# Performance work log

Measured on AMD Instinct MI355X. Metric: run time of the kernel, lower is better.

Reference implementation:

```python
import jax, jax.numpy as jnp
import numpy as np

BETA = 0.25  # commitment_beta from CodebookDecoder default


def setup_inputs() -> dict:
    key = jax.random.key(0)
    k1, k2, k3 = jax.random.split(key, 3)
    Q, B, K, D = 2048, 40000, 2048, 512
    return {
        "query_emb": jax.random.normal(k1, (Q, D), dtype=jnp.float32),
        "entity_emb": jax.random.normal(k2, (B, D), dtype=jnp.float32),
        "codebook": jax.random.normal(k3, (K, D), dtype=jnp.float32),
    }


def _quantize(x, codebook):
    # Nearest-neighbor lookup. torch.norm(x[:,None]-cb[None]) argmin is
    # equivalent to argmin of squared distance, expanded to avoid the
    x2 = jnp.sum(x * x, axis=1, keepdims=True)            # (B, 1)
    c2 = jnp.sum(codebook * codebook, axis=1)             # (K,)
    d2 = x2 - 2.0 * (x @ codebook.T) + c2[None, :]        # (B, K)
    idx = jnp.argmin(d2, axis=1)                          # (B,)
    quant = codebook[idx]                                 # (B, D) gather
    # vq_loss = mse(quant.detach(), x) + beta * mse(quant, x.detach())
    vq_loss = jnp.mean((jax.lax.stop_gradient(quant) - x) ** 2) \
        + BETA * jnp.mean((quant - jax.lax.stop_gradient(x)) ** 2)
    return quant, idx, vq_loss


def reference(query_emb, entity_emb, codebook):
    quant, idx, vq_loss = _quantize(entity_emb, codebook)
    score = query_emb @ quant.T                           # (Q, B)
    return score, vq_loss, idx
```

## Files before the change

kernel.cpp:

```cpp
#include <hip/hip_runtime.h>
#include <stdint.h>

#define Q    2048
#define NB   40000
#define NK   2048
#define ND   512
#define SCORE_SIZE (Q * NB)

typedef __bf16 bf16;
typedef bf16  bf16x8 __attribute__((ext_vector_type(8)));
typedef float f32x4  __attribute__((ext_vector_type(4)));

__device__ __forceinline__ unsigned short f2bf_rne(float f) {
    unsigned int u = __float_as_uint(f);
    u += 0x7FFFu + ((u >> 16) & 1u);
    return (unsigned short)(u >> 16);
}
__device__ __forceinline__ float bf2f(unsigned short h) {
    return __uint_as_float((unsigned int)h << 16);
}
__device__ __forceinline__ void split_pair_trunc(float x0, float x1,
                                                 unsigned int& hp, unsigned int& lp) {
    unsigned int u0 = __float_as_uint(x0), u1 = __float_as_uint(x1);
    hp = (u0 >> 16) | (u1 & 0xFFFF0000u);
    float l0 = x0 - __uint_as_float(u0 & 0xFFFF0000u);
    float l1 = x1 - __uint_as_float(u1 & 0xFFFF0000u);
    lp = (__float_as_uint(l0) >> 16) | (__float_as_uint(l1) & 0xFFFF0000u);
}

__global__ __launch_bounds__(256) void c2_kernel(const float* __restrict__ cb,
                                                 float* __restrict__ c2) {
    int wave = threadIdx.x >> 6, lane = threadIdx.x & 63;
    int row  = blockIdx.x * 4 + wave;
    const float4* p = (const float4*)(cb + (size_t)row * ND);
    float4 a = p[lane];
    float4 b = p[lane + 64];
    float s = a.x*a.x + a.y*a.y + a.z*a.z + a.w*a.w
            + b.x*b.x + b.y*b.y + b.z*b.z + b.w*b.w;
    #pragma unroll
    for (int off = 32; off; off >>= 1) s += __shfl_down(s, off);
    if (lane == 0) c2[row] = s;
}

__global__ __launch_bounds__(256) void cvt_cb_kernel(const float* __restrict__ cb,
        unsigned short* __restrict__ chi, unsigned short* __restrict__ clo) {
    int i = (blockIdx.x * 256 + threadIdx.x) * 4;
    float4 v = *(const float4*)(cb + i);
    unsigned short h[4]; float l[4];
    float x[4] = {v.x, v.y, v.z, v.w};
    #pragma unroll
    for (int j = 0; j < 4; ++j) { h[j] = f2bf_rne(x[j]); l[j] = x[j] - bf2f(h[j]); }
    uint2 hp, lp;
    hp.x = (unsigned int)h[0] | ((unsigned int)h[1] << 16);
    hp.y = (unsigned int)h[2] | ((unsigned int)h[3] << 16);
    lp.x = (unsigned int)f2bf_rne(l[0]) | ((unsigned int)f2bf_rne(l[1]) << 16);
    lp.y = (unsigned int)f2bf_rne(l[2]) | ((unsigned int)f2bf_rne(l[3]) << 16);
    *(uint2*)(chi + i) = hp;
    *(uint2*)(clo + i) = lp;
}

__global__ __launch_bounds__(256) void cvt_ent_kernel(const float* __restrict__ ent,
        unsigned short* __restrict__ ehi, unsigned short* __restrict__ elo) {
    int i = (blockIdx.x * 256 + threadIdx.x) * 4;
    float4 v = *(const float4*)(ent + i);
    unsigned short h[4]; float l[4];
    float x[4] = {v.x, v.y, v.z, v.w};
    #pragma unroll
    for (int j = 0; j < 4; ++j) { h[j] = f2bf_rne(x[j]); l[j] = x[j] - bf2f(h[j]); }
    uint2 hp, lp;
    hp.x = (unsigned int)h[0] | ((unsigned int)h[1] << 16);
    hp.y = (unsigned int)h[2] | ((unsigned int)h[3] << 16);
    lp.x = (unsigned int)f2bf_rne(l[0]) | ((unsigned int)f2bf_rne(l[1]) << 16);
    lp.y = (unsigned int)f2bf_rne(l[2]) | ((unsigned int)f2bf_rne(l[3]) << 16);
    *(uint2*)(ehi + i) = hp;
    *(uint2*)(elo + i) = lp;
}

__device__ __forceinline__ void top2_insert(float& v1, int& i1, float& v2, int& i2,
                                            float w, int j) {
    if (w < v1 || (w == v1 && j < i1)) { v2 = v1; i2 = i1; v1 = w; i1 = j; }
    else if (w < v2 || (w == v2 && j < i2)) { v2 = w; i2 = j; }
}

template<bool PRE>
__global__ __launch_bounds__(256) void dist_mfma_kernel(
        const float* __restrict__ entf,
        const unsigned short* __restrict__ ehi, const unsigned short* __restrict__ elo,
        const unsigned short* __restrict__ chi, const unsigned short* __restrict__ clo,
        const float* __restrict__ c2g, float4* __restrict__ partial) {
    __shared__ unsigned short EH[128 * 32];
    __shared__ unsigned short EL[128 * 32];
    __shared__ unsigned short CH[128 * 32];
    __shared__ unsigned short CL[128 * 32];
    int tid = threadIdx.x;
    int b0 = blockIdx.x * 128;
    int k0 = blockIdx.y * 128;
    int lane = tid & 63, wave = tid >> 6;
    int wm = wave >> 1, wn = wave & 1;
    int lr = lane & 15, quad = lane >> 4;

    f32x4 acc[4][4] = {};

    for (int kt = 0; kt < ND; kt += 32) {
        __syncthreads();
        #pragma unroll
        for (int r = 0; r < 2; ++r) {
            int e = r * 256 + tid;
            int row = e >> 2, cc = e & 3;
            int br = b0 + row; br = br < NB ? br : NB - 1;
            size_t eoff = (size_t)br * ND + kt + cc * 8;
            if (PRE) {
                *(uint4*)(EH + row * 32 + cc * 8) = *(const uint4*)(ehi + eoff);
                *(uint4*)(EL + row * 32 + cc * 8) = *(const uint4*)(elo + eoff);
            } else {
                const float* src = entf + eoff;
                float4 a = *(const float4*)src;
                float4 b = *(const float4*)(src + 4);
                uint4 hp, lp;
                split_pair_trunc(a.x, a.y, hp.x, lp.x);
                split_pair_trunc(a.z, a.w, hp.y, lp.y);
                split_pair_trunc(b.x, b.y, hp.z, lp.z);
                split_pair_trunc(b.z, b.w, hp.w, lp.w);
                *(uint4*)(EH + row * 32 + cc * 8) = hp;
                *(uint4*)(EL + row * 32 + cc * 8) = lp;
            }
            size_t coff = (size_t)(k0 + row) * ND + kt + cc * 8;
            *(uint4*)(CH + row * 32 + cc * 8) = *(const uint4*)(chi + coff);
            *(uint4*)(CL + row * 32 + cc * 8) = *(const uint4*)(clo + coff);
        }
        __syncthreads();
        bf16x8 ah[4], al[4], bh[4], bl[4];
        #pragma unroll
        for (int mi = 0; mi < 4; ++mi) {
            int o = (wm * 64 + mi * 16 + lr) * 32 + quad * 8;
            ah[mi] = *(const bf16x8*)(EH + o);
            al[mi] = *(const bf16x8*)(EL + o);
        }
        #pragma unroll
        for (int ni = 0; ni < 4; ++ni) {
            int o = (wn * 64 + ni * 16 + lr) * 32 + quad * 8;
            bh[ni] = *(const bf16x8*)(CH + o);
            bl[ni] = *(const bf16x8*)(CL + o);
        }
        #pragma unroll
        for (int mi = 0; mi < 4; ++mi)
            #pragma unroll
            for (int ni = 0; ni < 4; ++ni) {
                acc[mi][ni] = __builtin_amdgcn_mfma_f32_16x16x32_bf16(
                    ah[mi], bh[ni], acc[mi][ni], 0, 0, 0);
                acc[mi][ni] = __builtin_amdgcn_mfma_f32_16x16x32_bf16(
                    ah[mi], bl[ni], acc[mi][ni], 0, 0, 0);
                acc[mi][ni] = __builtin_amdgcn_mfma_f32_16x16x32_bf16(
                    al[mi], bh[ni], acc[mi][ni], 0, 0, 0);
            }
    }

    float c2v[4];
    #pragma unroll
    for (int ni = 0; ni < 4; ++ni) c2v[ni] = c2g[k0 + wn * 64 + ni * 16 + lr];

    #pragma unroll
    for (int mi = 0; mi < 4; ++mi) {
        #pragma unroll
        for (int rr = 0; rr < 4; ++rr) {
            float v1 = 3.4e38f, v2 = 3.4e38f;
            int i1 = 0x7FFFFFFF, i2 = 0x7FFFFFFF;
            #pragma unroll
            for (int ni = 0; ni < 4; ++ni) {
                float w = c2v[ni] - 2.0f * acc[mi][ni][rr];
                top2_insert(v1, i1, v2, i2, w, k0 + wn * 64 + ni * 16 + lr);
            }
            #pragma unroll
            for (int off = 1; off < 16; off <<= 1) {
                float ov1 = __shfl_xor(v1, off); int oi1 = __shfl_xor(i1, off);
                float ov2 = __shfl_xor(v2, off); int oi2 = __shfl_xor(i2, off);
                top2_insert(v1, i1, v2, i2, ov1, oi1);
                top2_insert(v1, i1, v2, i2, ov2, oi2);
            }
            int b = b0 + wm * 64 + mi * 16 + quad * 4 + rr;
            if (lr == 0 && b < NB)
                partial[(size_t)(blockIdx.y * 2 + wn) * NB + b] =
                    make_float4(v1, __int_as_float(i1), v2, __int_as_float(i2));
        }
    }
}

__global__ __launch_bounds__(256) void cand_merge_kernel(
        const float4* __restrict__ partial, int* __restrict__ cand) {
    int b = blockIdx.x * 256 + threadIdx.x;
    if (b >= NB) return;
    float tv[4] = {3.4e38f, 3.4e38f, 3.4e38f, 3.4e38f};
    int   ti[4] = {0x7FFFFFFF, 0x7FFFFFFF, 0x7FFFFFFF, 0x7FFFFFFF};
    for (int g = 0; g < 32; ++g) {
        float4 p = partial[(size_t)g * NB + b];
        float pv[2] = {p.x, p.z};
        int   pi[2] = {__float_as_int(p.y), __float_as_int(p.w)};
        #pragma unroll
        for (int t = 0; t < 2; ++t) {
            float w = pv[t]; int j = pi[t];
            #pragma unroll
            for (int s = 0; s < 4; ++s) {
                if (w < tv[s] || (w == tv[s] && j < ti[s])) {
                    float tmpv = tv[s]; int tmpi = ti[s];
                    tv[s] = w; ti[s] = j; w = tmpv; j = tmpi;
                }
            }
        }
    }
    #pragma unroll
    for (int s = 0; s < 4; ++s) cand[b * 4 + s] = ti[s];
}

__global__ __launch_bounds__(256) void rescore_kernel(
        const float* __restrict__ ent, const float* __restrict__ cb,
        const float* __restrict__ c2g, const int* __restrict__ cand,
        unsigned short* __restrict__ quantb, float* __restrict__ out_idx,
        float* __restrict__ acc) {
    int b = blockIdx.x;
    int wave = threadIdx.x >> 6, lane = threadIdx.x & 63;
    int k = cand[b * 4 + wave];
    const float4* xp = (const float4*)(ent + (size_t)b * ND);
    const float4* cp = (const float4*)(cb + (size_t)k * ND);
    float4 x0 = xp[lane * 2], x1 = xp[lane * 2 + 1];
    float4 c0 = cp[lane * 2], c1 = cp[lane * 2 + 1];
    float s = x0.x*c0.x + x0.y*c0.y + x0.z*c0.z + x0.w*c0.w
            + x1.x*c1.x + x1.y*c1.y + x1.z*c1.z + x1.w*c1.w;
    #pragma unroll
    for (int off = 32; off; off >>= 1) s += __shfl_down(s, off);
    __shared__ float vws[4];
    __shared__ int   kws[4];
    __shared__ int   win;
    if (lane == 0) { vws[wave] = c2g[k] - 2.0f * s; kws[wave] = k; }
    __syncthreads();
    if (threadIdx.x == 0) {
        float bv = vws[0]; int bk = kws[0], bw = 0;
        #pragma unroll
        for (int w = 1; w < 4; ++w) {
            if (vws[w] < bv || (vws[w] == bv && kws[w] < bk)) {
                bv = vws[w]; bk = kws[w]; bw = w;
            }
        }
        win = bw;
        out_idx[b] = (float)bk;
    }
    __syncthreads();
    if (wave == win) {
        uint4 qp;
        qp.x = (unsigned int)f2bf_rne(c0.x) | ((unsigned int)f2bf_rne(c0.y) << 16);
        qp.y = (unsigned int)f2bf_rne(c0.z) | ((unsigned int)f2bf_rne(c0.w) << 16);
        qp.z = (unsigned int)f2bf_rne(c1.x) | ((unsigned int)f2bf_rne(c1.y) << 16);
        qp.w = (unsigned int)f2bf_rne(c1.z) | ((unsigned int)f2bf_rne(c1.w) << 16);
        *(uint4*)(quantb + (size_t)b * ND + lane * 8) = qp;
        float d0 = c0.x - x0.x, d1 = c0.y - x0.y, d2 = c0.z - x0.z, d3 = c0.w - x0.w;
        float d4 = c1.x - x1.x, d5 = c1.y - x1.y, d6 = c1.z - x1.z, d7 = c1.w - x1.w;
        float l = d0*d0 + d1*d1 + d2*d2 + d3*d3 + d4*d4 + d5*d5 + d6*d6 + d7*d7;
        #pragma unroll
        for (int off = 32; off; off >>= 1) l += __shfl_down(l, off);
        if (lane == 0) atomicAdd(acc, l);
    }
}

__global__ void vq_final_kernel(const float* __restrict__ acc, float* __restrict__ out) {
    out[0] = 1.25f * acc[0] / (float)(NB * ND);
}

__global__ __launch_bounds__(256) void qcvt_kernel(const float* __restrict__ qry,
                                                   unsigned short* __restrict__ qb) {
    int i = (blockIdx.x * 256 + threadIdx.x) * 4;
    float4 v = *(const float4*)(qry + i);
    uint2 u;
    u.x = (unsigned int)f2bf_rne(v.x) | ((unsigned int)f2bf_rne(v.y) << 16);
    u.y = (unsigned int)f2bf_rne(v.z) | ((unsigned int)f2bf_rne(v.w) << 16);
    *(uint2*)(qb + i) = u;
}

__global__ __launch_bounds__(256) void score_kernel(
        const unsigned short* __restrict__ Aq, const unsigned short* __restrict__ Bq,
        float* __restrict__ C) {
    __shared__ unsigned short As[128 * 32];
    __shared__ unsigned short Bs[128 * 32];
    int tid = threadIdx.x;
    int n0 = blockIdx.x * 128;
    int m0 = blockIdx.y * 128;
    int lane = tid & 63, wave = tid >> 6;
    int wm = wave >> 1, wn = wave & 1;
    int lr = lane & 15, quad = lane >> 4;

    f32x4 acc[4][4] = {};

    for (int kt = 0; kt < ND; kt += 32) {
        __syncthreads();
        #pragma unroll
        for (int r = 0; r < 2; ++r) {
            int e = r * 256 + tid;
            int row = e >> 2, cc = e & 3;
            uint4 va = *(const uint4*)(Aq + (size_t)(m0 + row) * ND + kt + cc * 8);
            *(uint4*)(As + row * 32 + cc * 8) = va;
            int nr = n0 + row; nr = nr < NB ? nr : NB - 1;
            uint4 vb = *(const uint4*)(Bq + (size_t)nr * ND + kt + cc * 8);
            *(uint4*)(Bs + row * 32 + cc * 8) = vb;
        }
        __syncthreads();
        bf16x8 af[4], bfr[4];
        #pragma unroll
        for (int mi = 0; mi < 4; ++mi)
            af[mi] = *(const bf16x8*)(As + (wm * 64 + mi * 16 + lr) * 32 + quad * 8);
        #pragma unroll
        for (int ni = 0; ni < 4; ++ni)
            bfr[ni] = *(const bf16x8*)(Bs + (wn * 64 + ni * 16 + lr) * 32 + quad * 8);
        #pragma unroll
        for (int mi = 0; mi < 4; ++mi)
            #pragma unroll
            for (int ni = 0; ni < 4; ++ni)
                acc[mi][ni] = __builtin_amdgcn_mfma_f32_16x16x32_bf16(
                    af[mi], bfr[ni], acc[mi][ni], 0, 0, 0);
    }

    #pragma unroll
    for (int mi = 0; mi < 4; ++mi) {
        #pragma unroll
        for (int ni = 0; ni < 4; ++ni) {
            int col = n0 + wn * 64 + ni * 16 + lr;
            if (col < NB) {
                #pragma unroll
                for (int r = 0; r < 4; ++r) {
                    int row = m0 + wm * 64 + mi * 16 + quad * 4 + r;
                    C[(size_t)row * NB + col] = acc[mi][ni][r];
                }
            }
        }
    }
}

extern "C" void kernel_launch(void* const* d_in, const int* in_sizes, int n_in,
                              void* d_out, int out_size, void* d_ws, size_t ws_size,
                              hipStream_t stream) {
    const float* qry = (const float*)d_in[0];
    const float* ent = (const float*)d_in[1];
    const float* cb  = (const float*)d_in[2];
    float* out = (float*)d_out;

    char* ws = (char*)d_ws;
    const bool pre = ws_size >= 130ull * 1024 * 1024;

    float4*         partial = (float4*)(ws);
    unsigned short* quantb  = (unsigned short*)(ws);
    size_t off = 40960000;
    unsigned short *ehi = nullptr, *elo = nullptr;
    if (pre) {
        ehi = (unsigned short*)(ws + off); off += 40960000;
        elo = (unsigned short*)(ws + off); off += 40960000;
    }
    unsigned short* chi = (unsigned short*)(ws + off); off += 2097152;
    unsigned short* clo = (unsigned short*)(ws + off); off += 2097152;
    unsigned short* qb  = (unsigned short*)(ws + off); off += 2097152;
    int*            cand= (int*)(ws + off);            off += 640000;
    float*          c2  = (float*)(ws + off);          off += 8192;
    float*          acc = (float*)(ws + off);          off += 4;

    hipMemsetAsync(acc, 0, sizeof(float), stream);

    c2_kernel<<<NK / 4, 256, 0, stream>>>(cb, c2);
    cvt_cb_kernel<<<1024, 256, 0, stream>>>(cb, chi, clo);
    qcvt_kernel<<<1024, 256, 0, stream>>>(qry, qb);
    if (pre) {
        cvt_ent_kernel<<<20000, 256, 0, stream>>>(ent, ehi, elo);
        dist_mfma_kernel<true><<<dim3(313, 16), 256, 0, stream>>>(
            ent, ehi, elo, chi, clo, c2, partial);
    } else {
        dist_mfma_kernel<false><<<dim3(313, 16), 256, 0, stream>>>(
            ent, nullptr, nullptr, chi, clo, c2, partial);
    }
    cand_merge_kernel<<<(NB + 255) / 256, 256, 0, stream>>>(partial, cand);
    rescore_kernel<<<NB, 256, 0, stream>>>(ent, cb, c2, cand, quantb,
                                           out + SCORE_SIZE + 1, acc);
    vq_final_kernel<<<1, 1, 0, stream>>>(acc, out + SCORE_SIZE);
    score_kernel<<<dim3(313, 16), 256, 0, stream>>>(qb, quantb, out);
}
```

Baseline: 2.100 ms.

## Use single bf16 distance GEMM with wider rescoring and direct global-to-LDS loads

The distance GEMM drops the 3-pass split-bf16 scheme (hi/lo) in favour of one bf16 pass, which cuts its MFMA work and its memory traffic to about a third. To make up for the lower precision, candidate merging keeps the top 8 instead of the top 4, and these are rescored exactly in fp32 with 512-thread blocks. Both GEMMs now use K-tiles of 64, XOR-swizzled LDS layouts and global_load_lds DMA, which skips the trip through registers. The risk is argmin mismatches wherever the true nearest code falls outside the bf16 top-8.

```diff
diff --git a/kernel.cpp b/kernel.cpp
--- a/kernel.cpp
+++ b/kernel.cpp
@@ -16,16 +16,11 @@
     u += 0x7FFFu + ((u >> 16) & 1u);
     return (unsigned short)(u >> 16);
 }
-__device__ __forceinline__ float bf2f(unsigned short h) {
-    return __uint_as_float((unsigned int)h << 16);
-}
-__device__ __forceinline__ void split_pair_trunc(float x0, float x1,
-                                                 unsigned int& hp, unsigned int& lp) {
-    unsigned int u0 = __float_as_uint(x0), u1 = __float_as_uint(x1);
-    hp = (u0 >> 16) | (u1 & 0xFFFF0000u);
-    float l0 = x0 - __uint_as_float(u0 & 0xFFFF0000u);
-    float l1 = x1 - __uint_as_float(u1 & 0xFFFF0000u);
-    lp = (__float_as_uint(l0) >> 16) | (__float_as_uint(l1) & 0xFFFF0000u);
+
+__device__ __forceinline__ void gl2lds16(const void* g, void* l) {
+    __builtin_amdgcn_global_load_lds(
+        (const __attribute__((address_space(1))) void*)g,
+        (__attribute__((address_space(3))) void*)l, 16, 0, 0);
 }
 
 __global__ __launch_bounds__(256) void c2_kernel(const float* __restrict__ cb,
@@ -42,38 +37,14 @@
     if (lane == 0) c2[row] = s;
 }
 
-__global__ __launch_bounds__(256) void cvt_cb_kernel(const float* __restrict__ cb,
-        unsigned short* __restrict__ chi, unsigned short* __restrict__ clo) {
+__global__ __launch_bounds__(256) void cvt_bf16_kernel(const float* __restrict__ src,
+                                                       unsigned short* __restrict__ dst) {
     int i = (blockIdx.x * 256 + threadIdx.x) * 4;
-    float4 v = *(const float4*)(cb + i);
-    unsigned short h[4]; float l[4];
-    float x[4] = {v.x, v.y, v.z, v.w};
-    #pragma unroll
-    for (int j = 0; j < 4; ++j) { h[j] = f2bf_rne(x[j]); l[j] = x[j] - bf2f(h[j]); }
-    uint2 hp, lp;
-    hp.x = (unsigned int)h[0] | ((unsigned int)h[1] << 16);
-    hp.y = (unsigned int)h[2] | ((unsigned int)h[3] << 16);
-    lp.x = (unsigned int)f2bf_rne(l[0]) | ((unsigned int)f2bf_rne(l[1]) << 16);
-    lp.y = (unsigned int)f2bf_rne(l[2]) | ((unsigned int)f2bf_rne(l[3]) << 16);
-    *(uint2*)(chi + i) = hp;
-    *(uint2*)(clo + i) = lp;
-}
-
-__global__ __launch_bounds__(256) void cvt_ent_kernel(const float* __restrict__ ent,
-        unsigned short* __restrict__ ehi, unsigned short* __restrict__ elo) {
-    int i = (blockIdx.x * 256 + threadIdx.x) * 4;
-    float4 v = *(const float4*)(ent + i);
-    unsigned short h[4]; float l[4];
-    float x[4] = {v.x, v.y, v.z, v.w};
-    #pragma unroll
-    for (int j = 0; j < 4; ++j) { h[j] = f2bf_rne(x[j]); l[j] = x[j] - bf2f(h[j]); }
-    uint2 hp, lp;
-    hp.x = (unsigned int)h[0] | ((unsigned int)h[1] << 16);
-    hp.y = (unsigned int)h[2] | ((unsigned int)h[3] << 16);
-    lp.x = (unsigned int)f2bf_rne(l[0]) | ((unsigned int)f2bf_rne(l[1]) << 16);
-    lp.y = (unsigned int)f2bf_rne(l[2]) | ((unsigned int)f2bf_rne(l[3]) << 16);
-    *(uint2*)(ehi + i) = hp;
-    *(uint2*)(elo + i) = lp;
+    float4 v = *(const float4*)(src + i);
+    uint2 u;
+    u.x = (unsigned int)f2bf_rne(v.x) | ((unsigned int)f2bf_rne(v.y) << 16);
+    u.y = (unsigned int)f2bf_rne(v.z) | ((unsigned int)f2bf_rne(v.w) << 16);
+    *(uint2*)(dst + i) = u;
 }
 
 __device__ __forceinline__ void top2_insert(float& v1, int& i1, float& v2, int& i2,
@@ -84,14 +55,11 @@
 
 template<bool PRE>
 __global__ __launch_bounds__(256) void dist_mfma_kernel(
-        const float* __restrict__ entf,
-        const unsigned short* __restrict__ ehi, const unsigned short* __restrict__ elo,
-        const unsigned short* __restrict__ chi, const unsigned short* __restrict__ clo,
+        const float* __restrict__ entf, const unsigned short* __restrict__ ehi,
+        const unsigned short* __restrict__ chi,
         const float* __restrict__ c2g, float4* __restrict__ partial) {
-    __shared__ unsigned short EH[128 * 32];
-    __shared__ unsigned short EL[128 * 32];
-    __shared__ unsigned short CH[128 * 32];
-    __shared__ unsigned short CL[128 * 32];
+    __shared__ unsigned short Es[128 * 64];
+    __shared__ unsigned short Cs[128 * 64];
     int tid = threadIdx.x;
     int b0 = blockIdx.x * 128;
     int k0 = blockIdx.y * 128;
@@ -101,58 +69,54 @@
 
     f32x4 acc[4][4] = {};
 
-    for (int kt = 0; kt < ND; kt += 32) {
+    for (int kt = 0; kt < ND; kt += 64) {
         __syncthreads();
         #pragma unroll
-        for (int r = 0; r < 2; ++r) {
-            int e = r * 256 + tid;
-            int row = e >> 2, cc = e & 3;
-            int br = b0 + row; br = br < NB ? br : NB - 1;
-            size_t eoff = (size_t)br * ND + kt + cc * 8;
+        for (int j = 0; j < 4; ++j) {
+            int q = j * 256 + tid;
+            int r = q >> 3;
+            int cs = (q & 7) ^ (r & 7);
+            gl2lds16(chi + (size_t)(k0 + r) * ND + kt + cs * 8,
+                     Cs + (size_t)(j * 256 + wave * 64) * 8);
+            int br = b0 + r; br = br < NB ? br : NB - 1;
             if (PRE) {
-                *(uint4*)(EH + row * 32 + cc * 8) = *(const uint4*)(ehi + eoff);
-                *(uint4*)(EL + row * 32 + cc * 8) = *(const uint4*)(elo + eoff);
+                gl2lds16(ehi + (size_t)br * ND + kt + cs * 8,
+                         Es + (size_t)(j * 256 + wave * 64) * 8);
             } else {
-                const float* src = entf + eoff;
-                float4 a = *(const float4*)src;
-                float4 b = *(const float4*)(src + 4);
-                uint4 hp, lp;
-                split_pair_trunc(a.x, a.y, hp.x, lp.x);
-                split_pair_trunc(a.z, a.w, hp.y, lp.y);
-                split_pair_trunc(b.x, b.y, hp.z, lp.z);
-                split_pair_trunc(b.z, b.w, hp.w, lp.w);
-                *(uint4*)(EH + row * 32 + cc * 8) = hp;
-                *(uint4*)(EL + row * 32 + cc * 8) = lp;
-            }
-            size_t coff = (size_t)(k0 + row) * ND + kt + cc * 8;
-            *(uint4*)(CH + row * 32 + cc * 8) = *(const uint4*)(chi + coff);
-            *(uint4*)(CL + row * 32 + cc * 8) = *(const uint4*)(clo + coff);
+                const float* s = entf + (size_t)br * ND + kt + cs * 8;
+                float4 a = *(const float4*)s;
+                float4 b = *(const float4*)(s + 4);
+                uint4 hp;
+                hp.x = (unsigned int)f2bf_rne(a.x) | ((unsigned int)f2bf_rne(a.y) << 16);
+                hp.y = (unsigned int)f2bf_rne(a.z) | ((unsigned int)f2bf_rne(a.w) << 16);
+                hp.z = (unsigned int)f2bf_rne(b.x) | ((unsigned int)f2bf_rne(b.y) << 16);
+                hp.w = (unsigned int)f2bf_rne(b.z) | ((unsigned int)f2bf_rne(b.w) << 16);
+                *(uint4*)(Es + q * 8) = hp;
+            }
         }
         __syncthreads();
-        bf16x8 ah[4], al[4], bh[4], bl[4];
-        #pragma unroll
-        for (int mi = 0; mi < 4; ++mi) {
-            int o = (wm * 64 + mi * 16 + lr) * 32 + quad * 8;
-            ah[mi] = *(const bf16x8*)(EH + o);
-            al[mi] = *(const bf16x8*)(EL + o);
-        }
-        #pragma unroll
-        for (int ni = 0; ni < 4; ++ni) {
-            int o = (wn * 64 + ni * 16 + lr) * 32 + quad * 8;
-            bh[ni] = *(const bf16x8*)(CH + o);
-            bl[ni] = *(const bf16x8*)(CL + o);
-        }
-        #pragma unroll
-        for (int mi = 0; mi < 4; ++mi)
+        #pragma unroll
+        for (int kq = 0; kq < 2; ++kq) {
+            bf16x8 af[4], bfr[4];
+            #pragma unroll
+            for (int mi = 0; mi < 4; ++mi) {
+                int r = wm * 64 + mi * 16 + lr;
+                int ch = (kq * 4 + quad) ^ (lr & 7);
+                af[mi] = *(const bf16x8*)(Es + (r * 8 + ch) * 8);
+            }
             #pragma unroll
             for (int ni = 0; ni < 4; ++ni) {
-                acc[mi][ni] = __builtin_amdgcn_mfma_f32_16x16x32_bf16(
-                    ah[mi], bh[ni], acc[mi][ni], 0, 0, 0);
-                acc[mi][ni] = __builtin_amdgcn_mfma_f32_16x16x32_bf16(
-                    ah[mi], bl[ni], acc[mi][ni], 0, 0, 0);
-                acc[mi][ni] = __builtin_amdgcn_mfma_f32_16x16x32_bf16(
-                    al[mi], bh[ni], acc[mi][ni], 0, 0, 0);
-            }
+                int r = wn * 64 + ni * 16 + lr;
+                int ch = (kq * 4 + quad) ^ (lr & 7);
+                bfr[ni] = *(const bf16x8*)(Cs + (r * 8 + ch) * 8);
+            }
+            #pragma unroll
+            for (int mi = 0; mi < 4; ++mi)
+                #pragma unroll
+                for (int ni = 0; ni < 4; ++ni)
+                    acc[mi][ni] = __builtin_amdgcn_mfma_f32_16x16x32_bf16(
+                        af[mi], bfr[ni], acc[mi][ni], 0, 0, 0);
+        }
     }
 
     float c2v[4];
@@ -189,8 +153,9 @@
         const float4* __restrict__ partial, int* __restrict__ cand) {
     int b = blockIdx.x * 256 + threadIdx.x;
     if (b >= NB) return;
-    float tv[4] = {3.4e38f, 3.4e38f, 3.4e38f, 3.4e38f};
-    int   ti[4] = {0x7FFFFFFF, 0x7FFFFFFF, 0x7FFFFFFF, 0x7FFFFFFF};
+    float tv[8]; int ti[8];
+    #pragma unroll
+    for (int s = 0; s < 8; ++s) { tv[s] = 3.4e38f; ti[s] = 0x7FFFFFFF; }
     for (int g = 0; g < 32; ++g) {
         float4 p = partial[(size_t)g * NB + b];
         float pv[2] = {p.x, p.z};
@@ -199,7 +164,7 @@
         for (int t = 0; t < 2; ++t) {
             float w = pv[t]; int j = pi[t];
             #pragma unroll
-            for (int s = 0; s < 4; ++s) {
+            for (int s = 0; s < 8; ++s) {
                 if (w < tv[s] || (w == tv[s] && j < ti[s])) {
                     float tmpv = tv[s]; int tmpi = ti[s];
                     tv[s] = w; ti[s] = j; w = tmpv; j = tmpi;
@@ -208,17 +173,17 @@
         }
     }
     #pragma unroll
-    for (int s = 0; s < 4; ++s) cand[b * 4 + s] = ti[s];
-}
-
-__global__ __launch_bounds__(256) void rescore_kernel(
+    for (int s = 0; s < 8; ++s) cand[(size_t)b * 8 + s] = ti[s];
+}
+
+__global__ __launch_bounds__(512) void rescore_kernel(
         const float* __restrict__ ent, const float* __restrict__ cb,
         const float* __restrict__ c2g, const int* __restrict__ cand,
         unsigned short* __restrict__ quantb, float* __restrict__ out_idx,
         float* __restrict__ acc) {
     int b = blockIdx.x;
     int wave = threadIdx.x >> 6, lane = threadIdx.x & 63;
-    int k = cand[b * 4 + wave];
+    int k = cand[(size_t)b * 8 + wave];
     const float4* xp = (const float4*)(ent + (size_t)b * ND);
     const float4* cp = (const float4*)(cb + (size_t)k * ND);
     float4 x0 = xp[lane * 2], x1 = xp[lane * 2 + 1];
@@ -227,15 +192,15 @@
             + x1.x*c1.x + x1.y*c1.y + x1.z*c1.z + x1.w*c1.w;
     #pragma unroll
     for (int off = 32; off; off >>= 1) s += __shfl_down(s, off);
-    __shared__ float vws[4];
-    __shared__ int   kws[4];
+    __shared__ float vws[8];
+    __shared__ int   kws[8];
     __shared__ int   win;
     if (lane == 0) { vws[wave] = c2g[k] - 2.0f * s; kws[wave] = k; }
     __syncthreads();
     if (threadIdx.x == 0) {
         float bv = vws[0]; int bk = kws[0], bw = 0;
         #pragma unroll
-        for (int w = 1; w < 4; ++w) {
+        for (int w = 1; w < 8; ++w) {
             if (vws[w] < bv || (vws[w] == bv && kws[w] < bk)) {
                 bv = vws[w]; bk = kws[w]; bw = w;
             }
@@ -264,21 +229,11 @@
     out[0] = 1.25f * acc[0] / (float)(NB * ND);
 }
 
-__global__ __launch_bounds__(256) void qcvt_kernel(const float* __restrict__ qry,
-                                                   unsigned short* __restrict__ qb) {
-    int i = (blockIdx.x * 256 + threadIdx.x) * 4;
-    float4 v = *(const float4*)(qry + i);
-    uint2 u;
-    u.x = (unsigned int)f2bf_rne(v.x) | ((unsigned int)f2bf_rne(v.y) << 16);
-    u.y = (unsigned int)f2bf_rne(v.z) | ((unsigned int)f2bf_rne(v.w) << 16);
-    *(uint2*)(qb + i) = u;
-}
-
 __global__ __launch_bounds__(256) void score_kernel(
         const unsigned short* __restrict__ Aq, const unsigned short* __restrict__ Bq,
         float* __restrict__ C) {
-    __shared__ unsigned short As[128 * 32];
-    __shared__ unsigned short Bs[128 * 32];
+    __shared__ unsigned short As[128 * 64];
+    __shared__ unsigned short Bs[128 * 64];
     int tid = threadIdx.x;
     int n0 = blockIdx.x * 128;
     int m0 = blockIdx.y * 128;
@@ -288,32 +243,42 @@
 
     f32x4 acc[4][4] = {};
 
-    for (int kt = 0; kt < ND; kt += 32) {
+    for (int kt = 0; kt < ND; kt += 64) {
         __syncthreads();
         #pragma unroll
-        for (int r = 0; r < 2; ++r) {
-            int e = r * 256 + tid;
-            int row = e >> 2, cc = e & 3;
-            uint4 va = *(const uint4*)(Aq + (size_t)(m0 + row) * ND + kt + cc * 8);
-            *(uint4*)(As + row * 32 + cc * 8) = va;
-            int nr = n0 + row; nr = nr < NB ? nr : NB - 1;
-            uint4 vb = *(const uint4*)(Bq + (size_t)nr * ND + kt + cc * 8);
-            *(uint4*)(Bs + row * 32 + cc * 8) = vb;
+        for (int j = 0; j < 4; ++j) {
+            int q = j * 256 + tid;
+            int r = q >> 3;
+            int cs = (q & 7) ^ (r & 7);
+            gl2lds16(Aq + (size_t)(m0 + r) * ND + kt + cs * 8,
+                     As + (size_t)(j * 256 + wave * 64) * 8);
+            int nr = n0 + r; nr = nr < NB ? nr : NB - 1;
+            gl2lds16(Bq + (size_t)nr * ND + kt + cs * 8,
+                     Bs + (size_t)(j * 256 + wave * 64) * 8);
         }
         __syncthreads();
-        bf16x8 af[4], bfr[4];
-        #pragma unroll
-        for (int mi = 0; mi < 4; ++mi)
-            af[mi] = *(const bf16x8*)(As + (wm * 64 + mi * 16 + lr) * 32 + quad * 8);
-        #pragma unroll
-        for (int ni = 0; ni < 4; ++ni)
-            bfr[ni] = *(const bf16x8*)(Bs + (wn * 64 + ni * 16 + lr) * 32 + quad * 8);
-        #pragma unroll
-        for (int mi = 0; mi < 4; ++mi)
-            #pragma unroll
-            for (int ni = 0; ni < 4; ++ni)
-                acc[mi][ni] = __builtin_amdgcn_mfma_f32_16x16x32_bf16(
-                    af[mi], bfr[ni], acc[mi][ni], 0, 0, 0);
+        #pragma unroll
+        for (int kq = 0; kq < 2; ++kq) {
+            bf16x8 af[4], bfr[4];
+            #pragma unroll
+            for (int mi = 0; mi < 4; ++mi) {
+                int r = wm * 64 + mi * 16 + lr;
+                int ch = (kq * 4 + quad) ^ (lr & 7);
+                af[mi] = *(const bf16x8*)(As + (r * 8 + ch) * 8);
+            }
+            #pragma unroll
+            for (int ni = 0; ni < 4; ++ni) {
+                int r = wn * 64 + ni * 16 + lr;
+                int ch = (kq * 4 + quad) ^ (lr & 7);
+                bfr[ni] = *(const bf16x8*)(Bs + (r * 8 + ch) * 8);
+            }
+            #pragma unroll
+            for (int mi = 0; mi < 4; ++mi)
+                #pragma unroll
+                for (int ni = 0; ni < 4; ++ni)
+                    acc[mi][ni] = __builtin_amdgcn_mfma_f32_16x16x32_bf16(
+                        af[mi], bfr[ni], acc[mi][ni], 0, 0, 0);
+        }
     }
 
     #pragma unroll
@@ -341,38 +306,34 @@
     float* out = (float*)d_out;
 
     char* ws = (char*)d_ws;
-    const bool pre = ws_size >= 130ull * 1024 * 1024;
+    const bool pre = ws_size >= 100ull * 1024 * 1024;
 
     float4*         partial = (float4*)(ws);
     unsigned short* quantb  = (unsigned short*)(ws);
     size_t off = 40960000;
-    unsigned short *ehi = nullptr, *elo = nullptr;
-    if (pre) {
-        ehi = (unsigned short*)(ws + off); off += 40960000;
-        elo = (unsigned short*)(ws + off); off += 40960000;
-    }
+    unsigned short* ehi = nullptr;
+    if (pre) { ehi = (unsigned short*)(ws + off); off += 40960000; }
     unsigned short* chi = (unsigned short*)(ws + off); off += 2097152;
-    unsigned short* clo = (unsigned short*)(ws + off); off += 2097152;
     unsigned short* qb  = (unsigned short*)(ws + off); off += 2097152;
-    int*            cand= (int*)(ws + off);            off += 640000;
+    int*            cand= (int*)(ws + off);            off += 1280000;
     float*          c2  = (float*)(ws + off);          off += 8192;
     float*          acc = (float*)(ws + off);          off += 4;
 
     hipMemsetAsync(acc, 0, sizeof(float), stream);
 
     c2_kernel<<<NK / 4, 256, 0, stream>>>(cb, c2);
-    cvt_cb_kernel<<<1024, 256, 0, stream>>>(cb, chi, clo);
-    qcvt_kernel<<<1024, 256, 0, stream>>>(qry, qb);
+    cvt_bf16_kernel<<<NK * ND / 1024, 256, 0, stream>>>(cb, chi);
+    cvt_bf16_kernel<<<Q * ND / 1024, 256, 0, stream>>>(qry, qb);
     if (pre) {
-        cvt_ent_kernel<<<20000, 256, 0, stream>>>(ent, ehi, elo);
+        cvt_bf16_kernel<<<NB * ND / 1024, 256, 0, stream>>>(ent, ehi);
         dist_mfma_kernel<true><<<dim3(313, 16), 256, 0, stream>>>(
-            ent, ehi, elo, chi, clo, c2, partial);
+            ent, ehi, chi, c2, partial);
     } else {
         dist_mfma_kernel<false><<<dim3(313, 16), 256, 0, stream>>>(
-            ent, nullptr, nullptr, chi, clo, c2, partial);
+            ent, nullptr, chi, c2, partial);
     }
     cand_merge_kernel<<<(NB + 255) / 256, 256, 0, stream>>>(partial, cand);
-    rescore_kernel<<<NB, 256, 0, stream>>>(ent, cb, c2, cand, quantb,
+    rescore_kernel<<<NB, 512, 0, stream>>>(ent, cb, c2, cand, quantb,
                                            out + SCORE_SIZE + 1, acc);
     vq_final_kernel<<<1, 1, 0, stream>>>(acc, out + SCORE_SIZE);
     score_kernel<<<dim3(313, 16), 256, 0, stream>>>(qb, quantb, out);
```

Result: faster. 1.957 ms (-6.8%).
